# Kernel optimization log

Measured on AMD Instinct MI355X. Metric: run time of the kernel, lower is better.

## Reference

```python
import jax, jax.numpy as jnp
import numpy as np
from jax import lax

_A = -0.75  # PyTorch bicubic coefficient


def _cubic_kernel(x):
    x = np.abs(x)
    return np.where(x <= 1.0, (_A + 2) * x**3 - (_A + 3) * x**2 + 1,
                    np.where(x < 2.0, _A * x**3 - 5 * _A * x**2 + 8 * _A * x - 4 * _A, 0.0))


def _cubic_mat(out_s, in_s):
    # align_corners=True bicubic interpolation matrix [out_s, in_s]
    i = np.arange(out_s)
    s = i * (in_s - 1) / (out_s - 1) if out_s > 1 else np.zeros(out_s)
    f = np.floor(s).astype(np.int64)
    t = s - f
    M = np.zeros((out_s, in_s), dtype=np.float32)
    for off in range(-1, 3):
        idx = np.clip(f + off, 0, in_s - 1)
        np.add.at(M, (i, idx), _cubic_kernel(t - off).astype(np.float32))
    return jnp.asarray(M)


def _bicubic_up(x, out_hw):
    Mh = _cubic_mat(out_hw[0], x.shape[-2])
    Mw = _cubic_mat(out_hw[1], x.shape[-1])
    y = jnp.einsum('Hh,bchw->bcHw', Mh, x)
    return jnp.einsum('Ww,bcHw->bcHW', Mw, y)


def _conv(x, w, b, pad=1):
    y = lax.conv_general_dilated(x, w, (1, 1), [(pad, pad), (pad, pad)],
                                 dimension_numbers=('NCHW', 'OIHW', 'NCHW'))
    return y + b[None, :, None, None]


def _pool(x):
    return lax.reduce_window(x, -jnp.inf, lax.max, (1, 1, 2, 2), (1, 1, 2, 2), 'VALID')


def _features(x, ws):
    # VGG19 feat1 = conv0+relu (64ch, full res); feat2 = conv2..conv14 (256ch, 1/4 res)
    x1 = jax.nn.relu(_conv(x, *ws[0]))
    h = jax.nn.relu(_conv(x1, *ws[1]))
    h = _pool(h)
    h = jax.nn.relu(_conv(h, *ws[2]))
    h = jax.nn.relu(_conv(h, *ws[3]))
    h = _pool(h)
    h = jax.nn.relu(_conv(h, *ws[4]))
    h = jax.nn.relu(_conv(h, *ws[5]))
    h = jax.nn.relu(_conv(h, *ws[6]))
    h = _bicubic_up(h, x1.shape[-2:])  # bicubic, align_corners=True
    return jnp.concatenate([x1, h], axis=1)  # 64 + 256 = 320 channels


def _forward(x_ref, x_template, w0, b0, w2, b2, w5, b5, w7, b7, w10, b10, w12, b12,
             w14, b14, coef_ref, coef_temp, fw1, fb1, fw2, fb2, fw3, fb3):
    ws = [(w0, b0), (w2, b2), (w5, b5), (w7, b7), (w10, b10), (w12, b12), (w14, b14)]
    fref = _features(x_ref, ws)
    ftem = _features(x_template, ws)
    # L2-normalize over channel dim
    fref = fref / (1e-8 + jnp.linalg.norm(fref, axis=1, keepdims=True))
    ftem = ftem / (1e-8 + jnp.linalg.norm(ftem, axis=1, keepdims=True))
    b, c, H, W = fref.shape
    fref = fref.reshape(b, c, H // 2, 2, W // 2, 2).mean(axis=(3, 5))
    # dense correlation volume
    dist = jnp.einsum('bcmn,bcpq->bmnpq', fref, ftem) / 320.0
    m, n, p, q = dist.shape[1:]
    dist = dist.reshape(b, m * n, p * q)
    # dual-axis softmax + sqrt combination (LoFTR-style)
    conf_ref = jax.nn.softmax(coef_ref * dist, axis=-2)
    conf_tmp = jax.nn.softmax(coef_temp * dist, axis=-1)
    confidence = jnp.sqrt(conf_ref * conf_tmp)
    conf_values, _ = lax.top_k(confidence, 5)  # [b, m*n, 5]
    conf = conf_values.reshape(b, m, n, 5).transpose(0, 3, 1, 2)
    # final head (dropout = identity in eval)
    h = jax.nn.relu(_conv(conf, fw1, fb1))
    h = jax.nn.relu(_conv(h, fw2, fb2))
    out = _conv(h, fw3, fb3, pad=0)
    out = _bicubic_up(out, x_ref.shape[-2:])
    return out


def setup_inputs() -> dict:
    key = jax.random.key(0)
    ks = jax.random.split(key, 16)
    B, H, W = 1, 128, 128

    def cw(k, o, i, s):
        return jax.random.normal(k, (o, i, s, s), jnp.float32) * (1.0 / np.sqrt(i * s * s))

    d = {
        'x_ref': jax.random.normal(ks[0], (B, 3, H, W), jnp.float32),
        'x_template': jax.random.normal(ks[1], (B, 3, H, W), jnp.float32),
        'w0': cw(ks[2], 64, 3, 3), 'b0': jnp.zeros((64,), jnp.float32),
        'w2': cw(ks[3], 64, 64, 3), 'b2': jnp.zeros((64,), jnp.float32),
        'w5': cw(ks[4], 128, 64, 3), 'b5': jnp.zeros((128,), jnp.float32),
        'w7': cw(ks[5], 128, 128, 3), 'b7': jnp.zeros((128,), jnp.float32),
        'w10': cw(ks[6], 256, 128, 3), 'b10': jnp.zeros((256,), jnp.float32),
        'w12': cw(ks[7], 256, 256, 3), 'b12': jnp.zeros((256,), jnp.float32),
        'w14': cw(ks[8], 256, 256, 3), 'b14': jnp.zeros((256,), jnp.float32),
        'coef_ref': jnp.float32(1.0), 'coef_temp': jnp.float32(1.0),
        # final head: weights_init_normal -> N(1/3, 0.02)
        'fw1': 1.0 / 3 + 0.02 * jax.random.normal(ks[9], (8, 5, 3, 3), jnp.float32),
        'fb1': 0.02 * jax.random.normal(ks[10], (8,), jnp.float32),
        'fw2': 1.0 / 3 + 0.02 * jax.random.normal(ks[11], (8, 8, 3, 3), jnp.float32),
        'fb2': 0.02 * jax.random.normal(ks[12], (8,), jnp.float32),
        'fw3': 1.0 / 3 + 0.02 * jax.random.normal(ks[13], (1, 8, 1, 1), jnp.float32),
        'fb3': 0.02 * jax.random.normal(ks[14], (1,), jnp.float32),
    }
    return d


def reference(x_ref, x_template, w0, b0, w2, b2, w5, b5, w7, b7, w10, b10, w12, b12,
              w14, b14, coef_ref, coef_temp, fw1, fb1, fw2, fb2, fw3, fb3):
    return _forward(x_ref, x_template, w0, b0, w2, b2, w5, b5, w7, b7, w10, b10,
                    w12, b12, w14, b14, coef_ref, coef_temp, fw1, fb1, fw2, fb2, fw3, fb3)
```

## Files before the change

kernel.cpp:

```cpp
#include <hip/hip_runtime.h>
#include <math.h>

typedef unsigned short ushort_t;
typedef unsigned int uint_t;
typedef __attribute__((ext_vector_type(8))) short bf16x8;
typedef __attribute__((ext_vector_type(4))) float f32x4;

#define FSTRIDE ((size_t)16384 * 320)
#define TSTRIDE ((size_t)16384 * 64)

__device__ inline ushort_t f2bf(float f) {
    union { float f; uint_t u; } x; x.f = f;
    uint_t r = x.u + 0x7fffu + ((x.u >> 16) & 1u);
    return (ushort_t)(r >> 16);
}
__device__ inline float bf2f(ushort_t h) {
    union { uint_t u; float f; } x; x.u = ((uint_t)h) << 16;
    return x.f;
}
__device__ inline float bflo(uint_t u) {
    union { uint_t u; float f; } x; x.u = u << 16; return x.f;
}
__device__ inline float bfhi(uint_t u) {
    union { uint_t u; float f; } x; x.u = u & 0xffff0000u; return x.f;
}
__device__ inline uint_t cvtpk_bf16(float lo, float hi) {
    uint_t r;
    asm volatile("v_cvt_pk_bf16_f32 %0, %1, %2" : "=v"(r) : "v"(lo), "v"(hi));
    return r;
}
__device__ inline void gload16(const void* g, void* l) {
    __builtin_amdgcn_global_load_lds(
        (const __attribute__((address_space(1))) void*)g,
        (__attribute__((address_space(3))) void*)l, 16, 0, 0);
}

__global__ void wtrans_k(const float* __restrict__ w, ushort_t* __restrict__ wT, int CO, int CI)
{
    int idx = blockIdx.x * 256 + threadIdx.x;
    if (idx >= CO * CI * 9) return;
    int tap = idx % 9;
    int rem = idx / 9;
    int ci = rem % CI;
    int co = rem / CI;
    wT[((size_t)tap * CO + co) * CI + ci] = f2bf(w[idx]);
}

__global__ __launch_bounds__(256) void conv0_k(const float* __restrict__ x0, const float* __restrict__ x1,
                                               const float* __restrict__ w,
                                               const float* __restrict__ b, ushort_t* __restrict__ F)
{
    const float* x = blockIdx.y ? x1 : x0;
    F += (size_t)blockIdx.y * FSTRIDE;
    int co = threadIdx.x & 63;
    int p = blockIdx.x * 4 + (threadIdx.x >> 6);
    int y = p >> 7, xx = p & 127;
    float acc = b[co];
#pragma unroll
    for (int ci = 0; ci < 3; ++ci) {
#pragma unroll
        for (int t = 0; t < 9; ++t) {
            int dy = t / 3 - 1, dx = t % 3 - 1;
            int yy = y + dy, xc = xx + dx;
            if ((unsigned)yy < 128u && (unsigned)xc < 128u) {
                acc += x[ci * 16384 + yy * 128 + xc] * w[co * 27 + ci * 9 + t];
            }
        }
    }
    F[(size_t)p * 320 + co] = f2bf(fmaxf(acc, 0.f));
}

template<int CI>
__global__ __launch_bounds__(256) void conv_mfma_k(
    const ushort_t* __restrict__ in, int ldin, int inoff, size_t inImgStride,
    const ushort_t* __restrict__ wT, const float* __restrict__ bias,
    ushort_t* __restrict__ out, int ldout, int outoff, size_t outImgStride,
    int H, int W, int CO)
{
    in += (size_t)blockIdx.z * inImgStride;
    out += (size_t)blockIdx.z * outImgStride;
    const int tid = threadIdx.x;
    const int lane = tid & 63, wid = tid >> 6;
    const int wr = wid >> 1, wc = wid & 1;
    const int m0 = blockIdx.x * 64;
    const int n0 = blockIdx.y * 64;
    const int fr = lane & 15;
    const int fo = (lane >> 4) << 3;

    size_t abase[2];
    unsigned vmask[2];
#pragma unroll
    for (int mi = 0; mi < 2; ++mi) {
        int p = m0 + wr * 32 + mi * 16 + fr;
        int y = p / W, x = p % W;
        abase[mi] = (size_t)p * ldin + inoff + fo;
        unsigned vm = 0;
#pragma unroll
        for (int t = 0; t < 9; ++t) {
            int dy = t / 3 - 1, dx = t % 3 - 1;
            if ((unsigned)(y + dy) < (unsigned)H && (unsigned)(x + dx) < (unsigned)W) vm |= 1u << t;
        }
        vmask[mi] = vm;
    }

    f32x4 zero = {0.f, 0.f, 0.f, 0.f};
    f32x4 acc[2][2] = {{zero, zero}, {zero, zero}};
    const bf16x8 zz = {0, 0, 0, 0, 0, 0, 0, 0};

    for (int t = 0; t < 9; ++t) {
        int toff = ((t / 3 - 1) * W + (t % 3 - 1)) * ldin;
        bool v0 = (vmask[0] >> t) & 1u;
        bool v1 = (vmask[1] >> t) & 1u;
        const ushort_t* wp0 = wT + ((size_t)(t * CO + n0 + wc * 32 + fr)) * CI + fo;
        const ushort_t* wp1 = wp0 + (size_t)16 * CI;
#pragma unroll
        for (int kc = 0; kc < CI / 32; ++kc) {
            int k0 = kc * 32;
            bf16x8 a0 = v0 ? *(const bf16x8*)(in + abase[0] + toff + k0) : zz;
            bf16x8 a1 = v1 ? *(const bf16x8*)(in + abase[1] + toff + k0) : zz;
            bf16x8 b0 = *(const bf16x8*)(wp0 + k0);
            bf16x8 b1 = *(const bf16x8*)(wp1 + k0);
            acc[0][0] = __builtin_amdgcn_mfma_f32_16x16x32_bf16(b0, a0, acc[0][0], 0, 0, 0);
            acc[0][1] = __builtin_amdgcn_mfma_f32_16x16x32_bf16(b1, a0, acc[0][1], 0, 0, 0);
            acc[1][0] = __builtin_amdgcn_mfma_f32_16x16x32_bf16(b0, a1, acc[1][0], 0, 0, 0);
            acc[1][1] = __builtin_amdgcn_mfma_f32_16x16x32_bf16(b1, a1, acc[1][1], 0, 0, 0);
        }
    }

#pragma unroll
    for (int mi = 0; mi < 2; ++mi) {
#pragma unroll
        for (int ni = 0; ni < 2; ++ni) {
            int pix = m0 + wr * 32 + mi * 16 + (lane & 15);
            int ch = n0 + wc * 32 + ni * 16 + ((lane >> 4) << 2);
            float4 bv = *(const float4*)(bias + ch);
            float r0 = fmaxf(acc[mi][ni][0] + bv.x, 0.f);
            float r1 = fmaxf(acc[mi][ni][1] + bv.y, 0.f);
            float r2 = fmaxf(acc[mi][ni][2] + bv.z, 0.f);
            float r3 = fmaxf(acc[mi][ni][3] + bv.w, 0.f);
            uint2 pk;
            pk.x = (uint_t)f2bf(r0) | ((uint_t)f2bf(r1) << 16);
            pk.y = (uint_t)f2bf(r2) | ((uint_t)f2bf(r3) << 16);
            *(uint2*)(out + (size_t)pix * ldout + outoff + ch) = pk;
        }
    }
}

template<int CI>
__global__ __launch_bounds__(64) void conv_mfma1w_k(
    const ushort_t* __restrict__ in, int ldin, size_t inImgStride,
    const ushort_t* __restrict__ wT, const float* __restrict__ bias,
    ushort_t* __restrict__ out, int ldout, size_t outImgStride,
    int H, int W, int CO)
{
    in += (size_t)blockIdx.z * inImgStride;
    out += (size_t)blockIdx.z * outImgStride;
    const int lane = threadIdx.x;
    const int m0 = blockIdx.x * 32;
    const int n0 = blockIdx.y * 32;
    const int fr = lane & 15;
    const int fo = (lane >> 4) << 3;

    size_t abase[2];
    unsigned vmask[2];
#pragma unroll
    for (int mi = 0; mi < 2; ++mi) {
        int p = m0 + mi * 16 + fr;
        int y = p / W, x = p % W;
        abase[mi] = (size_t)p * ldin + fo;
        unsigned vm = 0;
#pragma unroll
        for (int t = 0; t < 9; ++t) {
            int dy = t / 3 - 1, dx = t % 3 - 1;
            if ((unsigned)(y + dy) < (unsigned)H && (unsigned)(x + dx) < (unsigned)W) vm |= 1u << t;
        }
        vmask[mi] = vm;
    }

    f32x4 zero = {0.f, 0.f, 0.f, 0.f};
    f32x4 acc[2][2] = {{zero, zero}, {zero, zero}};
    const bf16x8 zz = {0, 0, 0, 0, 0, 0, 0, 0};

    for (int t = 0; t < 9; ++t) {
        int toff = ((t / 3 - 1) * W + (t % 3 - 1)) * ldin;
        bool v0 = (vmask[0] >> t) & 1u;
        bool v1 = (vmask[1] >> t) & 1u;
        const ushort_t* wp0 = wT + ((size_t)(t * CO + n0 + fr)) * CI + fo;
        const ushort_t* wp1 = wp0 + (size_t)16 * CI;
#pragma unroll
        for (int kc = 0; kc < CI / 32; ++kc) {
            int k0 = kc * 32;
            bf16x8 a0 = v0 ? *(const bf16x8*)(in + abase[0] + toff + k0) : zz;
            bf16x8 a1 = v1 ? *(const bf16x8*)(in + abase[1] + toff + k0) : zz;
            bf16x8 b0 = *(const bf16x8*)(wp0 + k0);
            bf16x8 b1 = *(const bf16x8*)(wp1 + k0);
            acc[0][0] = __builtin_amdgcn_mfma_f32_16x16x32_bf16(b0, a0, acc[0][0], 0, 0, 0);
            acc[0][1] = __builtin_amdgcn_mfma_f32_16x16x32_bf16(b1, a0, acc[0][1], 0, 0, 0);
            acc[1][0] = __builtin_amdgcn_mfma_f32_16x16x32_bf16(b0, a1, acc[1][0], 0, 0, 0);
            acc[1][1] = __builtin_amdgcn_mfma_f32_16x16x32_bf16(b1, a1, acc[1][1], 0, 0, 0);
        }
    }

#pragma unroll
    for (int mi = 0; mi < 2; ++mi) {
#pragma unroll
        for (int ni = 0; ni < 2; ++ni) {
            int pix = m0 + mi * 16 + (lane & 15);
            int ch = n0 + ni * 16 + ((lane >> 4) << 2);
            float4 bv = *(const float4*)(bias + ch);
            float r0 = fmaxf(acc[mi][ni][0] + bv.x, 0.f);
            float r1 = fmaxf(acc[mi][ni][1] + bv.y, 0.f);
            float r2 = fmaxf(acc[mi][ni][2] + bv.z, 0.f);
            float r3 = fmaxf(acc[mi][ni][3] + bv.w, 0.f);
            uint2 pk;
            pk.x = (uint_t)f2bf(r0) | ((uint_t)f2bf(r1) << 16);
            pk.y = (uint_t)f2bf(r2) | ((uint_t)f2bf(r3) << 16);
            *(uint2*)(out + (size_t)pix * ldout + ch) = pk;
        }
    }
}

__global__ void maxpool_nhwc_k(const ushort_t* __restrict__ in, ushort_t* __restrict__ out,
                               int C, int Hi, int Wi)
{
    in += (size_t)blockIdx.y * TSTRIDE;
    out += (size_t)blockIdx.y * TSTRIDE;
    int idx = blockIdx.x * 256 + threadIdx.x;
    int CG = C >> 3;
    int Wo = Wi >> 1, Ho = Hi >> 1;
    if (idx >= Ho * Wo * CG) return;
    int cg = idx % CG;
    int p = idx / CG;
    int y = p / Wo, x = p % Wo;
    const ushort_t* ip = in + ((size_t)(2 * y) * Wi + 2 * x) * C + cg * 8;
    bf16x8 v0 = *(const bf16x8*)(ip);
    bf16x8 v1 = *(const bf16x8*)(ip + C);
    bf16x8 v2 = *(const bf16x8*)(ip + (size_t)Wi * C);
    bf16x8 v3 = *(const bf16x8*)(ip + (size_t)Wi * C + C);
    bf16x8 r;
#pragma unroll
    for (int j = 0; j < 8; ++j) {
        float m = fmaxf(fmaxf(bf2f((ushort_t)v0[j]), bf2f((ushort_t)v1[j])),
                        fmaxf(bf2f((ushort_t)v2[j]), bf2f((ushort_t)v3[j])));
        r[j] = (short)f2bf(m);
    }
    *(bf16x8*)(out + (size_t)p * C + cg * 8) = r;
}

__device__ inline void cubw(float t, float* w) {
    float x0 = 1.f + t, x2 = 1.f - t, x3 = 2.f - t;
    w[0] = ((-0.75f*x0 + 3.75f)*x0 - 6.f)*x0 + 3.f;
    w[1] = (1.25f*t - 2.25f)*t*t + 1.f;
    w[2] = (1.25f*x2 - 2.25f)*x2*x2 + 1.f;
    w[3] = ((-0.75f*x3 + 3.75f)*x3 - 6.f)*x3 + 3.f;
}

__global__ __launch_bounds__(256) void bicubic_nhwc_k(const ushort_t* __restrict__ in, ushort_t* __restrict__ F)
{
    in += (size_t)blockIdx.y * TSTRIDE;
    F += (size_t)blockIdx.y * FSTRIDE;
    int idx = blockIdx.x * 256 + threadIdx.x;
    int cg = idx & 31;
    int p = idx >> 5;
    int Y = p >> 7, X = p & 127;
    float sy = (float)Y * (31.f / 127.f);
    float sx = (float)X * (31.f / 127.f);
    int fy = (int)floorf(sy), fx = (int)floorf(sx);
    float ty = sy - (float)fy, tx = sx - (float)fx;
    float wy[4], wx[4];
    cubw(ty, wy); cubw(tx, wx);
    float a[8] = {0.f, 0.f, 0.f, 0.f, 0.f, 0.f, 0.f, 0.f};
#pragma unroll
    for (int i = 0; i < 4; ++i) {
        int yy = min(max(fy - 1 + i, 0), 31);
#pragma unroll
        for (int j = 0; j < 4; ++j) {
            int xx = min(max(fx - 1 + j, 0), 31);
            float w = wy[i] * wx[j];
            bf16x8 v = *(const bf16x8*)(in + ((size_t)yy * 32 + xx) * 256 + cg * 8);
#pragma unroll
            for (int e = 0; e < 8; ++e) a[e] += w * bf2f((ushort_t)v[e]);
        }
    }
    bf16x8 r;
#pragma unroll
    for (int e = 0; e < 8; ++e) r[e] = (short)f2bf(a[e]);
    *(bf16x8*)(F + (size_t)p * 320 + 64 + cg * 8) = r;
}

__global__ __launch_bounds__(256) void norm_k(ushort_t* __restrict__ F)
{
    int lane = threadIdx.x & 63;
    int p = blockIdx.x * 4 + (threadIdx.x >> 6);
    ushort_t* rp = F + (size_t)p * 320;
    bool act = lane < 40;
    bf16x8 v = {0, 0, 0, 0, 0, 0, 0, 0};
    float ss = 0.f;
    if (act) {
        v = *(const bf16x8*)(rp + lane * 8);
#pragma unroll
        for (int e = 0; e < 8; ++e) { float f = bf2f((ushort_t)v[e]); ss += f * f; }
    }
#pragma unroll
    for (int off = 32; off > 0; off >>= 1) ss += __shfl_xor(ss, off);
    float inv = 1.f / (1e-8f + sqrtf(ss));
    if (act) {
#pragma unroll
        for (int e = 0; e < 8; ++e) v[e] = (short)f2bf(bf2f((ushort_t)v[e]) * inv);
        *(bf16x8*)(rp + lane * 8) = v;
    }
}

__global__ void pool_ref_nhwc_k(const ushort_t* __restrict__ F, ushort_t* __restrict__ A)
{
    int idx = blockIdx.x * 256 + threadIdx.x;
    if (idx >= 4096 * 40) return;
    int cg = idx % 40;
    int m = idx / 40;
    int y = m >> 6, x = m & 63;
    const ushort_t* ip = F + ((size_t)(2 * y) * 128 + 2 * x) * 320 + cg * 8;
    bf16x8 v0 = *(const bf16x8*)(ip);
    bf16x8 v1 = *(const bf16x8*)(ip + 320);
    bf16x8 v2 = *(const bf16x8*)(ip + 128 * 320);
    bf16x8 v3 = *(const bf16x8*)(ip + 128 * 320 + 320);
    bf16x8 r;
#pragma unroll
    for (int j = 0; j < 8; ++j) {
        float s = bf2f((ushort_t)v0[j]) + bf2f((ushort_t)v1[j]) + bf2f((ushort_t)v2[j]) + bf2f((ushort_t)v3[j]);
        r[j] = (short)f2bf(0.25f * s);
    }
    *(bf16x8*)(A + (size_t)m * 320 + cg * 8) = r;
}

__global__ __launch_bounds__(256) void gemm_corr_k(
    const ushort_t* __restrict__ A, const ushort_t* __restrict__ B, ushort_t* __restrict__ D,
    const float* __restrict__ coefr, const float* __restrict__ coeft,
    float* __restrict__ rpsum, float* __restrict__ cpsum)
{
    __shared__ ushort_t lA[128 * 32];
    __shared__ ushort_t lB[128 * 32];
    __shared__ float cl[2][128];
    __shared__ float rl[2][128];
    const int tid = threadIdx.x;
    const int lane = tid & 63;
    const int wid = tid >> 6;
    const int wr = wid >> 1, wc = wid & 1;
    const int m0 = blockIdx.y * 128, n0 = blockIdx.x * 128;
    const int fr = lane & 15;
    const int fo = (lane >> 4) << 3;
    const int srow = tid >> 2;
    const int scol = (tid & 3) << 3;

    const ushort_t* Ag0 = A + (size_t)(m0 + srow) * 320 + scol;
    const ushort_t* Ag1 = Ag0 + (size_t)64 * 320;
    const ushort_t* Bg0 = B + (size_t)(n0 + srow) * 320 + scol;
    const ushort_t* Bg1 = Bg0 + (size_t)64 * 320;
    ushort_t* lA0 = lA + wid * 512;
    ushort_t* lA1 = lA + 2048 + wid * 512;
    ushort_t* lB0 = lB + wid * 512;
    ushort_t* lB1 = lB + 2048 + wid * 512;

    f32x4 zero = {0.f, 0.f, 0.f, 0.f};
    f32x4 acc[4][4];
#pragma unroll
    for (int i = 0; i < 4; ++i)
#pragma unroll
        for (int j = 0; j < 4; ++j) acc[i][j] = zero;

    for (int k0 = 0; k0 < 320; k0 += 32) {
        gload16(Ag0 + k0, lA0);
        gload16(Ag1 + k0, lA1);
        gload16(Bg0 + k0, lB0);
        gload16(Bg1 + k0, lB1);
        __syncthreads();
        bf16x8 af[4], bfr[4];
#pragma unroll
        for (int mi = 0; mi < 4; ++mi)
            af[mi] = *(const bf16x8*)&lA[(wr * 64 + mi * 16 + fr) * 32 + fo];
#pragma unroll
        for (int ni = 0; ni < 4; ++ni)
            bfr[ni] = *(const bf16x8*)&lB[(wc * 64 + ni * 16 + fr) * 32 + fo];
#pragma unroll
        for (int mi = 0; mi < 4; ++mi)
#pragma unroll
            for (int ni = 0; ni < 4; ++ni)
                acc[mi][ni] = __builtin_amdgcn_mfma_f32_16x16x32_bf16(bfr[ni], af[mi], acc[mi][ni], 0, 0, 0);
        __syncthreads();
    }

    const float s = 1.0f / 320.0f;
    const float cr = coefr[0], ct = coeft[0];
    const bool sameCoef = (cr == ct);
    float rpx[4] = {0.f, 0.f, 0.f, 0.f};
    float cpx[4][4];
#pragma unroll
    for (int ni = 0; ni < 4; ++ni)
#pragma unroll
        for (int r = 0; r < 4; ++r) cpx[ni][r] = 0.f;

    const int mrow = lane & 15;
    const int ng = (lane >> 4) << 2;
#pragma unroll
    for (int mi = 0; mi < 4; ++mi) {
        int m = m0 + wr * 64 + mi * 16 + mrow;
        ushort_t* drow = D + (size_t)m * 16384;
#pragma unroll
        for (int ni = 0; ni < 4; ++ni) {
            int n = n0 + wc * 64 + ni * 16 + ng;
            float d0 = acc[mi][ni][0] * s;
            float d1 = acc[mi][ni][1] * s;
            float d2 = acc[mi][ni][2] * s;
            float d3 = acc[mi][ni][3] * s;
            uint2 pk;
            pk.x = cvtpk_bf16(d0, d1);
            pk.y = cvtpk_bf16(d2, d3);
            *(uint2*)(drow + n) = pk;
            float e0 = __expf(cr * d0), e1 = __expf(cr * d1);
            float e2 = __expf(cr * d2), e3 = __expf(cr * d3);
            cpx[ni][0] += e0; cpx[ni][1] += e1; cpx[ni][2] += e2; cpx[ni][3] += e3;
            if (sameCoef) {
                rpx[mi] += e0 + e1 + e2 + e3;
            } else {
                rpx[mi] += __expf(ct * d0) + __expf(ct * d1) + __expf(ct * d2) + __expf(ct * d3);
            }
        }
    }
#pragma unroll
    for (int mi = 0; mi < 4; ++mi) {
        rpx[mi] += __shfl_xor(rpx[mi], 16);
        rpx[mi] += __shfl_xor(rpx[mi], 32);
    }
    if (lane < 16) {
#pragma unroll
        for (int mi = 0; mi < 4; ++mi)
            rl[wc][wr * 64 + mi * 16 + lane] = rpx[mi];
    }
#pragma unroll
    for (int ni = 0; ni < 4; ++ni)
#pragma unroll
        for (int r = 0; r < 4; ++r) {
            cpx[ni][r] += __shfl_xor(cpx[ni][r], 1);
            cpx[ni][r] += __shfl_xor(cpx[ni][r], 2);
            cpx[ni][r] += __shfl_xor(cpx[ni][r], 4);
            cpx[ni][r] += __shfl_xor(cpx[ni][r], 8);
        }
    if ((lane & 15) == 0) {
        int g = lane >> 4;
#pragma unroll
        for (int ni = 0; ni < 4; ++ni)
#pragma unroll
            for (int r = 0; r < 4; ++r)
                cl[wr][wc * 64 + ni * 16 + g * 4 + r] = cpx[ni][r];
    }
    __syncthreads();
    if (tid < 128) {
        cpsum[(size_t)blockIdx.y * 16384 + n0 + tid] = cl[0][tid] + cl[1][tid];
        rpsum[(size_t)blockIdx.x * 4096 + m0 + tid] = rl[0][tid] + rl[1][tid];
    }
}

__global__ void colfin_k(const float* __restrict__ cpsum, float* __restrict__ lc)
{
    int j = blockIdx.x * 256 + threadIdx.x;
    float s = 0.f;
#pragma unroll
    for (int k = 0; k < 32; ++k) s += cpsum[(size_t)k * 16384 + j];
    lc[j] = -0.5f * __logf(s);
}
__global__ void rowfin_k(const float* __restrict__ rpsum, float* __restrict__ invr)
{
    int m = blockIdx.x * 256 + threadIdx.x;
    float s = 0.f;
#pragma unroll
    for (int k = 0; k < 128; ++k) s += rpsum[(size_t)k * 4096 + m];
    invr[m] = rsqrtf(s);
}

#define INS5(w_) { float w = (w_); float mx; \
    mx = fmaxf(w, t0); w = fminf(w, t0); t0 = mx; \
    mx = fmaxf(w, t1); w = fminf(w, t1); t1 = mx; \
    mx = fmaxf(w, t2); w = fminf(w, t2); t2 = mx; \
    mx = fmaxf(w, t3); w = fminf(w, t3); t3 = mx; \
    t4 = fmaxf(w, t4); }

__global__ __launch_bounds__(256) void row_topk_k(
    const ushort_t* __restrict__ Dist, const float* __restrict__ lc,
    const float* __restrict__ invr,
    const float* __restrict__ coefr, const float* __restrict__ coeft,
    float* __restrict__ conf5)
{
    int wid = threadIdx.x >> 6, lane = threadIdx.x & 63;
    int row = blockIdx.x * 4 + wid;
    float hc = 0.5f * (coefr[0] + coeft[0]);
    const ushort_t* rp = Dist + (size_t)row * 16384;

    float t0 = -1e30f, t1 = -1e30f, t2 = -1e30f, t3 = -1e30f, t4 = -1e30f;
    for (int i = 0; i < 32; ++i) {
        int col = (i * 64 + lane) * 8;
        uint4 u = *(const uint4*)(rp + col);
        float4 l0 = *(const float4*)(lc + col);
        float4 l1 = *(const float4*)(lc + col + 4);
        INS5(fmaf(hc, bflo(u.x), l0.x));
        INS5(fmaf(hc, bfhi(u.x), l0.y));
        INS5(fmaf(hc, bflo(u.y), l0.z));
        INS5(fmaf(hc, bfhi(u.y), l0.w));
        INS5(fmaf(hc, bflo(u.z), l1.x));
        INS5(fmaf(hc, bfhi(u.z), l1.y));
        INS5(fmaf(hc, bflo(u.w), l1.z));
        INS5(fmaf(hc, bfhi(u.w), l1.w));
    }
#pragma unroll
    for (int off = 1; off < 64; off <<= 1) {
        float o0 = __shfl_xor(t0, off), o1 = __shfl_xor(t1, off), o2 = __shfl_xor(t2, off);
        float o3 = __shfl_xor(t3, off), o4 = __shfl_xor(t4, off);
        INS5(o0); INS5(o1); INS5(o2); INS5(o3); INS5(o4);
    }
    if (lane == 0) {
        float iv = invr[row];
        conf5[0 * 4096 + row] = __expf(t0) * iv;
        conf5[1 * 4096 + row] = __expf(t1) * iv;
        conf5[2 * 4096 + row] = __expf(t2) * iv;
        conf5[3 * 4096 + row] = __expf(t3) * iv;
        conf5[4 * 4096 + row] = __expf(t4) * iv;
    }
}

__global__ void conv3x3_k(const float* __restrict__ in, const float* __restrict__ wgt,
                          const float* __restrict__ bias, float* __restrict__ out,
                          int Cin, int H, int W, int relu)
{
    int p = blockIdx.x * 256 + threadIdx.x;
    int HW = H * W;
    if (p >= HW) return;
    int co0 = blockIdx.y * 8;
    int y = p / W, x = p - y * W;
    float acc0 = bias[co0+0], acc1 = bias[co0+1], acc2 = bias[co0+2], acc3 = bias[co0+3];
    float acc4 = bias[co0+4], acc5 = bias[co0+5], acc6 = bias[co0+6], acc7 = bias[co0+7];
    bool ym = y > 0, yp = y < H-1, xm = x > 0, xp = x < W-1;
    for (int ci = 0; ci < Cin; ++ci) {
        const float* ip = in + (size_t)ci * HW + p;
        float v0 = (ym && xm) ? ip[-W-1] : 0.f;
        float v1 = (ym)       ? ip[-W]   : 0.f;
        float v2 = (ym && xp) ? ip[-W+1] : 0.f;
        float v3 = (xm)       ? ip[-1]   : 0.f;
        float v4 =              ip[0];
        float v5 = (xp)       ? ip[1]    : 0.f;
        float v6 = (yp && xm) ? ip[W-1]  : 0.f;
        float v7 = (yp)       ? ip[W]    : 0.f;
        float v8 = (yp && xp) ? ip[W+1]  : 0.f;
        const float* wp = wgt + ((size_t)co0 * Cin + ci) * 9;
        size_t ws = (size_t)Cin * 9;
#define CACC(q, a) { const float* wq = wp + q * ws; \
        a += wq[0]*v0 + wq[1]*v1 + wq[2]*v2 + wq[3]*v3 + wq[4]*v4 \
           + wq[5]*v5 + wq[6]*v6 + wq[7]*v7 + wq[8]*v8; }
        CACC(0, acc0) CACC(1, acc1) CACC(2, acc2) CACC(3, acc3)
        CACC(4, acc4) CACC(5, acc5) CACC(6, acc6) CACC(7, acc7)
#undef CACC
    }
#define CW(q, a) { float r = a; if (relu) r = fmaxf(r, 0.f); out[(size_t)(co0+q)*HW + p] = r; }
    CW(0, acc0) CW(1, acc1) CW(2, acc2) CW(3, acc3)
    CW(4, acc4) CW(5, acc5) CW(6, acc6) CW(7, acc7)
#undef CW
}

__global__ void bicubic_k(const float* __restrict__ in, float* __restrict__ out,
                          int C, int Hin, int Win, int Hout, int Wout)
{
    int idx = blockIdx.x * 256 + threadIdx.x;
    int total = C * Hout * Wout;
    if (idx >= total) return;
    int X = idx % Wout;
    int Y = (idx / Wout) % Hout;
    int c = idx / (Wout * Hout);
    float sy = (float)Y * (float)(Hin - 1) / (float)(Hout - 1);
    float sx = (float)X * (float)(Win - 1) / (float)(Wout - 1);
    int fy = (int)floorf(sy), fx = (int)floorf(sx);
    float ty = sy - (float)fy, tx = sx - (float)fx;
    float wy[4], wx[4];
    cubw(ty, wy); cubw(tx, wx);
    const float* ip = in + (size_t)c * Hin * Win;
    float acc = 0.f;
#pragma unroll
    for (int i = 0; i < 4; ++i) {
        int yy = min(max(fy - 1 + i, 0), Hin - 1);
        float ra = 0.f;
#pragma unroll
        for (int j = 0; j < 4; ++j) {
            int xx = min(max(fx - 1 + j, 0), Win - 1);
            ra += wx[j] * ip[yy * Win + xx];
        }
        acc += wy[i] * ra;
    }
    out[idx] = acc;
}

__global__ void conv1x1_k(const float* __restrict__ in, const float* __restrict__ w,
                          const float* __restrict__ b, float* __restrict__ out, int Cin, int HW)
{
    int p = blockIdx.x * 256 + threadIdx.x;
    if (p >= HW) return;
    float a = b[0];
    for (int c = 0; c < Cin; ++c) a += w[c] * in[(size_t)c * HW + p];
    out[p] = a;
}

extern "C" void kernel_launch(void* const* d_in, const int* in_sizes, int n_in,
                              void* d_out, int out_size, void* d_ws, size_t ws_size,
                              hipStream_t stream)
{
    const float* x_ref = (const float*)d_in[0];
    const float* x_tem = (const float*)d_in[1];
    const float* w0  = (const float*)d_in[2];   const float* b0  = (const float*)d_in[3];
    const float* w2  = (const float*)d_in[4];   const float* b2  = (const float*)d_in[5];
    const float* w5  = (const float*)d_in[6];   const float* b5  = (const float*)d_in[7];
    const float* w7  = (const float*)d_in[8];   const float* b7  = (const float*)d_in[9];
    const float* w10 = (const float*)d_in[10];  const float* b10 = (const float*)d_in[11];
    const float* w12 = (const float*)d_in[12];  const float* b12 = (const float*)d_in[13];
    const float* w14 = (const float*)d_in[14];  const float* b14 = (const float*)d_in[15];
    const float* coefr = (const float*)d_in[16];
    const float* coeft = (const float*)d_in[17];
    const float* fw1 = (const float*)d_in[18];  const float* fb1 = (const float*)d_in[19];
    const float* fw2 = (const float*)d_in[20];  const float* fb2 = (const float*)d_in[21];
    const float* fw3 = (const float*)d_in[22];  const float* fb3 = (const float*)d_in[23];
    float* out = (float*)d_out;

    char* wsp = (char*)d_ws;
    auto alloc = [&](size_t bytes) { char* p = wsp; wsp += (bytes + 255) & ~(size_t)255; return p; };
    ushort_t* F     = (ushort_t*)alloc(2 * FSTRIDE * 2);
    ushort_t* t1    = (ushort_t*)alloc(2 * TSTRIDE * 2);
    ushort_t* t2    = (ushort_t*)alloc(2 * TSTRIDE * 2);
    ushort_t* wT2   = (ushort_t*)alloc((size_t)64 * 64 * 9 * 2);
    ushort_t* wT5   = (ushort_t*)alloc((size_t)128 * 64 * 9 * 2);
    ushort_t* wT7   = (ushort_t*)alloc((size_t)128 * 128 * 9 * 2);
    ushort_t* wT10  = (ushort_t*)alloc((size_t)256 * 128 * 9 * 2);
    ushort_t* wT12  = (ushort_t*)alloc((size_t)256 * 256 * 9 * 2);
    ushort_t* wT14  = (ushort_t*)alloc((size_t)256 * 256 * 9 * 2);
    ushort_t* Abuf  = (ushort_t*)alloc((size_t)4096 * 320 * 2);
    ushort_t* dist  = (ushort_t*)alloc((size_t)4096 * 16384 * 2);
    float*    rpsum = (float*)alloc((size_t)128 * 4096 * 4);
    float*    cpsum = (float*)alloc((size_t)32 * 16384 * 4);
    float*    lc    = (float*)alloc(16384 * 4);
    float*    invr  = (float*)alloc(4096 * 4);
    float*    conf5 = (float*)alloc(5 * 4096 * 4);
    float*    h1    = (float*)alloc(8 * 4096 * 4);
    float*    h2    = (float*)alloc(8 * 4096 * 4);
    float*    out64 = (float*)alloc(4096 * 4);
    (void)ws_size; (void)n_in; (void)in_sizes; (void)out_size;

    wtrans_k<<<(64*64*9 + 255)/256, 256, 0, stream>>>(w2, wT2, 64, 64);
    wtrans_k<<<(128*64*9 + 255)/256, 256, 0, stream>>>(w5, wT5, 128, 64);
    wtrans_k<<<(128*128*9 + 255)/256, 256, 0, stream>>>(w7, wT7, 128, 128);
    wtrans_k<<<(256*128*9 + 255)/256, 256, 0, stream>>>(w10, wT10, 256, 128);
    wtrans_k<<<(256*256*9 + 255)/256, 256, 0, stream>>>(w12, wT12, 256, 256);
    wtrans_k<<<(256*256*9 + 255)/256, 256, 0, stream>>>(w14, wT14, 256, 256);

    conv0_k<<<dim3(4096, 2), 256, 0, stream>>>(x_ref, x_tem, w0, b0, F);
    conv_mfma_k<64><<<dim3(256, 1, 2), 256, 0, stream>>>(F, 320, 0, FSTRIDE, wT2, b2, t1, 64, 0, TSTRIDE, 128, 128, 64);
    maxpool_nhwc_k<<<dim3(128, 2), 256, 0, stream>>>(t1, t2, 64, 128, 128);
    conv_mfma_k<64><<<dim3(64, 2, 2), 256, 0, stream>>>(t2, 64, 0, TSTRIDE, wT5, b5, t1, 128, 0, TSTRIDE, 64, 64, 128);
    conv_mfma_k<128><<<dim3(64, 2, 2), 256, 0, stream>>>(t1, 128, 0, TSTRIDE, wT7, b7, t2, 128, 0, TSTRIDE, 64, 64, 128);
    maxpool_nhwc_k<<<dim3(64, 2), 256, 0, stream>>>(t2, t1, 128, 64, 64);
    conv_mfma1w_k<128><<<dim3(32, 8, 2), 64, 0, stream>>>(t1, 128, TSTRIDE, wT10, b10, t2, 256, TSTRIDE, 32, 32, 256);
    conv_mfma1w_k<256><<<dim3(32, 8, 2), 64, 0, stream>>>(t2, 256, TSTRIDE, wT12, b12, t1, 256, TSTRIDE, 32, 32, 256);
    conv_mfma1w_k<256><<<dim3(32, 8, 2), 64, 0, stream>>>(t1, 256, TSTRIDE, wT14, b14, t2, 256, TSTRIDE, 32, 32, 256);
    bicubic_nhwc_k<<<dim3(2048, 2), 256, 0, stream>>>(t2, F);
    norm_k<<<8192, 256, 0, stream>>>(F);

    pool_ref_nhwc_k<<<640, 256, 0, stream>>>(F, Abuf);

    gemm_corr_k<<<dim3(128, 32), 256, 0, stream>>>(Abuf, F + FSTRIDE, dist, coefr, coeft, rpsum, cpsum);

    colfin_k<<<64, 256, 0, stream>>>(cpsum, lc);
    rowfin_k<<<16, 256, 0, stream>>>(rpsum, invr);

    row_topk_k<<<1024, 256, 0, stream>>>(dist, lc, invr, coefr, coeft, conf5);

    conv3x3_k<<<dim3(16, 1), 256, 0, stream>>>(conf5, fw1, fb1, h1, 5, 64, 64, 1);
    conv3x3_k<<<dim3(16, 1), 256, 0, stream>>>(h1, fw2, fb2, h2, 8, 64, 64, 1);
    conv1x1_k<<<16, 256, 0, stream>>>(h2, fw3, fb3, out64, 8, 4096);
    bicubic_k<<<64, 256, 0, stream>>>(out64, out, 1, 64, 64, 128, 128);
}
```

Measured before the change: 409.7 us.

## Fuse small kernels, prefetch GEMM tiles via registers, early-exit top-k insert

```diff
diff --git a/kernel.cpp b/kernel.cpp
--- a/kernel.cpp
+++ b/kernel.cpp
@@ -29,21 +29,26 @@
     asm volatile("v_cvt_pk_bf16_f32 %0, %1, %2" : "=v"(r) : "v"(lo), "v"(hi));
     return r;
 }
-__device__ inline void gload16(const void* g, void* l) {
-    __builtin_amdgcn_global_load_lds(
-        (const __attribute__((address_space(1))) void*)g,
-        (__attribute__((address_space(3))) void*)l, 16, 0, 0);
-}
-
-__global__ void wtrans_k(const float* __restrict__ w, ushort_t* __restrict__ wT, int CO, int CI)
-{
-    int idx = blockIdx.x * 256 + threadIdx.x;
+
+struct WT6 {
+    const float* src[6];
+    ushort_t* dst[6];
+    int co[6], ci[6];
+    int off[6];
+};
+__global__ void wtrans6_k(WT6 a)
+{
+    int b = blockIdx.x, seg = 0;
+#pragma unroll
+    for (int s = 1; s < 6; ++s) if (b >= a.off[s]) seg = s;
+    int idx = (b - a.off[seg]) * 256 + threadIdx.x;
+    int CO = a.co[seg], CI = a.ci[seg];
     if (idx >= CO * CI * 9) return;
     int tap = idx % 9;
     int rem = idx / 9;
     int ci = rem % CI;
     int co = rem / CI;
-    wT[((size_t)tap * CO + co) * CI + ci] = f2bf(w[idx]);
+    a.dst[seg][((size_t)tap * CO + co) * CI + ci] = f2bf(a.src[seg][idx]);
 }
 
 __global__ __launch_bounds__(256) void conv0_k(const float* __restrict__ x0, const float* __restrict__ x1,
@@ -255,13 +260,12 @@
     w[3] = ((-0.75f*x3 + 3.75f)*x3 - 6.f)*x3 + 3.f;
 }
 
-__global__ __launch_bounds__(256) void bicubic_nhwc_k(const ushort_t* __restrict__ in, ushort_t* __restrict__ F)
+__global__ __launch_bounds__(256) void upnorm_k(const ushort_t* __restrict__ in, ushort_t* __restrict__ F)
 {
     in += (size_t)blockIdx.y * TSTRIDE;
     F += (size_t)blockIdx.y * FSTRIDE;
-    int idx = blockIdx.x * 256 + threadIdx.x;
-    int cg = idx & 31;
-    int p = idx >> 5;
+    int wid = threadIdx.x >> 6, lane = threadIdx.x & 63;
+    int p = blockIdx.x * 4 + wid;
     int Y = p >> 7, X = p & 127;
     float sy = (float)Y * (31.f / 127.f);
     float sx = (float)X * (31.f / 127.f);
@@ -269,7 +273,7 @@
     float ty = sy - (float)fy, tx = sx - (float)fx;
     float wy[4], wx[4];
     cubw(ty, wy); cubw(tx, wx);
-    float a[8] = {0.f, 0.f, 0.f, 0.f, 0.f, 0.f, 0.f, 0.f};
+    float a0 = 0.f, a1 = 0.f, a2 = 0.f, a3 = 0.f;
 #pragma unroll
     for (int i = 0; i < 4; ++i) {
         int yy = min(max(fy - 1 + i, 0), 31);
@@ -277,38 +281,22 @@
         for (int j = 0; j < 4; ++j) {
             int xx = min(max(fx - 1 + j, 0), 31);
             float w = wy[i] * wx[j];
-            bf16x8 v = *(const bf16x8*)(in + ((size_t)yy * 32 + xx) * 256 + cg * 8);
-#pragma unroll
-            for (int e = 0; e < 8; ++e) a[e] += w * bf2f((ushort_t)v[e]);
-        }
-    }
-    bf16x8 r;
-#pragma unroll
-    for (int e = 0; e < 8; ++e) r[e] = (short)f2bf(a[e]);
-    *(bf16x8*)(F + (size_t)p * 320 + 64 + cg * 8) = r;
-}
-
-__global__ __launch_bounds__(256) void norm_k(ushort_t* __restrict__ F)
-{
-    int lane = threadIdx.x & 63;
-    int p = blockIdx.x * 4 + (threadIdx.x >> 6);
-    ushort_t* rp = F + (size_t)p * 320;
-    bool act = lane < 40;
-    bf16x8 v = {0, 0, 0, 0, 0, 0, 0, 0};
-    float ss = 0.f;
-    if (act) {
-        v = *(const bf16x8*)(rp + lane * 8);
-#pragma unroll
-        for (int e = 0; e < 8; ++e) { float f = bf2f((ushort_t)v[e]); ss += f * f; }
-    }
+            uint2 v = *(const uint2*)(in + ((size_t)yy * 32 + xx) * 256 + lane * 4);
+            a0 += w * bflo(v.x); a1 += w * bfhi(v.x);
+            a2 += w * bflo(v.y); a3 += w * bfhi(v.y);
+        }
+    }
+    float v0 = bf2f(f2bf(a0)), v1 = bf2f(f2bf(a1)), v2 = bf2f(f2bf(a2)), v3 = bf2f(f2bf(a3));
+    float c0 = bf2f(F[(size_t)p * 320 + lane]);
+    float ss = c0 * c0 + v0 * v0 + v1 * v1 + v2 * v2 + v3 * v3;
 #pragma unroll
     for (int off = 32; off > 0; off >>= 1) ss += __shfl_xor(ss, off);
     float inv = 1.f / (1e-8f + sqrtf(ss));
-    if (act) {
-#pragma unroll
-        for (int e = 0; e < 8; ++e) v[e] = (short)f2bf(bf2f((ushort_t)v[e]) * inv);
-        *(bf16x8*)(rp + lane * 8) = v;
-    }
+    F[(size_t)p * 320 + lane] = f2bf(c0 * inv);
+    uint2 pk;
+    pk.x = (uint_t)f2bf(v0 * inv) | ((uint_t)f2bf(v1 * inv) << 16);
+    pk.y = (uint_t)f2bf(v2 * inv) | ((uint_t)f2bf(v3 * inv) << 16);
+    *(uint2*)(F + (size_t)p * 320 + 64 + lane * 4) = pk;
 }
 
 __global__ void pool_ref_nhwc_k(const ushort_t* __restrict__ F, ushort_t* __restrict__ A)
@@ -355,10 +343,6 @@
     const ushort_t* Ag1 = Ag0 + (size_t)64 * 320;
     const ushort_t* Bg0 = B + (size_t)(n0 + srow) * 320 + scol;
     const ushort_t* Bg1 = Bg0 + (size_t)64 * 320;
-    ushort_t* lA0 = lA + wid * 512;
-    ushort_t* lA1 = lA + 2048 + wid * 512;
-    ushort_t* lB0 = lB + wid * 512;
-    ushort_t* lB1 = lB + 2048 + wid * 512;
 
     f32x4 zero = {0.f, 0.f, 0.f, 0.f};
     f32x4 acc[4][4];
@@ -367,11 +351,27 @@
 #pragma unroll
         for (int j = 0; j < 4; ++j) acc[i][j] = zero;
 
-    for (int k0 = 0; k0 < 320; k0 += 32) {
-        gload16(Ag0 + k0, lA0);
-        gload16(Ag1 + k0, lA1);
-        gload16(Bg0 + k0, lB0);
-        gload16(Bg1 + k0, lB1);
+    uint4 ra0[2], ra1[2], rb0[2], rb1[2];
+    ra0[0] = *(const uint4*)(Ag0);
+    ra1[0] = *(const uint4*)(Ag1);
+    rb0[0] = *(const uint4*)(Bg0);
+    rb1[0] = *(const uint4*)(Bg1);
+
+#pragma unroll
+    for (int t = 0; t < 10; ++t) {
+        const int cs = t & 1, ns = cs ^ 1;
+        __syncthreads();
+        *(uint4*)&lA[srow * 32 + scol] = ra0[cs];
+        *(uint4*)&lA[(64 + srow) * 32 + scol] = ra1[cs];
+        *(uint4*)&lB[srow * 32 + scol] = rb0[cs];
+        *(uint4*)&lB[(64 + srow) * 32 + scol] = rb1[cs];
+        if (t < 9) {
+            int kk = 32 * (t + 1);
+            ra0[ns] = *(const uint4*)(Ag0 + kk);
+            ra1[ns] = *(const uint4*)(Ag1 + kk);
+            rb0[ns] = *(const uint4*)(Bg0 + kk);
+            rb1[ns] = *(const uint4*)(Bg1 + kk);
+        }
         __syncthreads();
         bf16x8 af[4], bfr[4];
 #pragma unroll
@@ -385,7 +385,6 @@
 #pragma unroll
             for (int ni = 0; ni < 4; ++ni)
                 acc[mi][ni] = __builtin_amdgcn_mfma_f32_16x16x32_bf16(bfr[ni], af[mi], acc[mi][ni], 0, 0, 0);
-        __syncthreads();
     }
 
     const float s = 1.0f / 320.0f;
@@ -459,21 +458,23 @@
     }
 }
 
-__global__ void colfin_k(const float* __restrict__ cpsum, float* __restrict__ lc)
-{
-    int j = blockIdx.x * 256 + threadIdx.x;
-    float s = 0.f;
-#pragma unroll
-    for (int k = 0; k < 32; ++k) s += cpsum[(size_t)k * 16384 + j];
-    lc[j] = -0.5f * __logf(s);
-}
-__global__ void rowfin_k(const float* __restrict__ rpsum, float* __restrict__ invr)
-{
-    int m = blockIdx.x * 256 + threadIdx.x;
-    float s = 0.f;
-#pragma unroll
-    for (int k = 0; k < 128; ++k) s += rpsum[(size_t)k * 4096 + m];
-    invr[m] = rsqrtf(s);
+__global__ void finboth_k(const float* __restrict__ cpsum, const float* __restrict__ rpsum,
+                          float* __restrict__ lc, float* __restrict__ invr)
+{
+    int b = blockIdx.x;
+    if (b < 64) {
+        int j = b * 256 + threadIdx.x;
+        float s = 0.f;
+#pragma unroll
+        for (int k = 0; k < 32; ++k) s += cpsum[(size_t)k * 16384 + j];
+        lc[j] = -0.5f * __logf(s);
+    } else {
+        int m = (b - 64) * 256 + threadIdx.x;
+        float s = 0.f;
+#pragma unroll
+        for (int k = 0; k < 128; ++k) s += rpsum[(size_t)k * 4096 + m];
+        invr[m] = rsqrtf(s);
+    }
 }
 
 #define INS5(w_) { float w = (w_); float mx; \
@@ -500,14 +501,20 @@
         uint4 u = *(const uint4*)(rp + col);
         float4 l0 = *(const float4*)(lc + col);
         float4 l1 = *(const float4*)(lc + col + 4);
-        INS5(fmaf(hc, bflo(u.x), l0.x));
-        INS5(fmaf(hc, bfhi(u.x), l0.y));
-        INS5(fmaf(hc, bflo(u.y), l0.z));
-        INS5(fmaf(hc, bfhi(u.y), l0.w));
-        INS5(fmaf(hc, bflo(u.z), l1.x));
-        INS5(fmaf(hc, bfhi(u.z), l1.y));
-        INS5(fmaf(hc, bflo(u.w), l1.z));
-        INS5(fmaf(hc, bfhi(u.w), l1.w));
+        float k0 = fmaf(hc, bflo(u.x), l0.x);
+        float k1 = fmaf(hc, bfhi(u.x), l0.y);
+        float k2 = fmaf(hc, bflo(u.y), l0.z);
+        float k3 = fmaf(hc, bfhi(u.y), l0.w);
+        float k4 = fmaf(hc, bflo(u.z), l1.x);
+        float k5 = fmaf(hc, bfhi(u.z), l1.y);
+        float k6 = fmaf(hc, bflo(u.w), l1.z);
+        float k7 = fmaf(hc, bfhi(u.w), l1.w);
+        float m8 = fmaxf(fmaxf(fmaxf(k0, k1), fmaxf(k2, k3)),
+                         fmaxf(fmaxf(k4, k5), fmaxf(k6, k7)));
+        if (m8 > t4) {
+            INS5(k0); INS5(k1); INS5(k2); INS5(k3);
+            INS5(k4); INS5(k5); INS5(k6); INS5(k7);
+        }
     }
 #pragma unroll
     for (int off = 1; off < 64; off <<= 1) {
@@ -563,6 +570,41 @@
 #undef CW
 }
 
+__global__ void head2_k(const float* __restrict__ in, const float* __restrict__ wgt,
+                        const float* __restrict__ bias, const float* __restrict__ w3,
+                        const float* __restrict__ b3, float* __restrict__ out64)
+{
+    int p = blockIdx.x * 256 + threadIdx.x;
+    int y = p >> 6, x = p & 63;
+    float acc[8];
+#pragma unroll
+    for (int c = 0; c < 8; ++c) acc[c] = bias[c];
+    bool ym = y > 0, yp = y < 63, xm = x > 0, xp = x < 63;
+#pragma unroll
+    for (int ci = 0; ci < 8; ++ci) {
+        const float* ip = in + ci * 4096 + p;
+        float v0 = (ym && xm) ? ip[-65] : 0.f;
+        float v1 = (ym)       ? ip[-64] : 0.f;
+        float v2 = (ym && xp) ? ip[-63] : 0.f;
+        float v3 = (xm)       ? ip[-1]  : 0.f;
+        float v4 =              ip[0];
+        float v5 = (xp)       ? ip[1]   : 0.f;
+        float v6 = (yp && xm) ? ip[63]  : 0.f;
+        float v7 = (yp)       ? ip[64]  : 0.f;
+        float v8 = (yp && xp) ? ip[65]  : 0.f;
+#pragma unroll
+        for (int co = 0; co < 8; ++co) {
+            const float* wq = wgt + ((size_t)co * 8 + ci) * 9;
+            acc[co] += wq[0]*v0 + wq[1]*v1 + wq[2]*v2 + wq[3]*v3 + wq[4]*v4
+                     + wq[5]*v5 + wq[6]*v6 + wq[7]*v7 + wq[8]*v8;
+        }
+    }
+    float o = b3[0];
+#pragma unroll
+    for (int c = 0; c < 8; ++c) o += w3[c] * fmaxf(acc[c], 0.f);
+    out64[p] = o;
+}
+
 __global__ void bicubic_k(const float* __restrict__ in, float* __restrict__ out,
                           int C, int Hin, int Win, int Hout, int Wout)
 {
@@ -592,16 +634,6 @@
         acc += wy[i] * ra;
     }
     out[idx] = acc;
-}
-
-__global__ void conv1x1_k(const float* __restrict__ in, const float* __restrict__ w,
-                          const float* __restrict__ b, float* __restrict__ out, int Cin, int HW)
-{
-    int p = blockIdx.x * 256 + threadIdx.x;
-    if (p >= HW) return;
-    float a = b[0];
-    for (int c = 0; c < Cin; ++c) a += w[c] * in[(size_t)c * HW + p];
-    out[p] = a;
 }
 
 extern "C" void kernel_launch(void* const* d_in, const int* in_sizes, int n_in,
@@ -643,16 +675,19 @@
     float*    invr  = (float*)alloc(4096 * 4);
     float*    conf5 = (float*)alloc(5 * 4096 * 4);
     float*    h1    = (float*)alloc(8 * 4096 * 4);
-    float*    h2    = (float*)alloc(8 * 4096 * 4);
     float*    out64 = (float*)alloc(4096 * 4);
     (void)ws_size; (void)n_in; (void)in_sizes; (void)out_size;
 
-    wtrans_k<<<(64*64*9 + 255)/256, 256, 0, stream>>>(w2, wT2, 64, 64);
-    wtrans_k<<<(128*64*9 + 255)/256, 256, 0, stream>>>(w5, wT5, 128, 64);
-    wtrans_k<<<(128*128*9 + 255)/256, 256, 0, stream>>>(w7, wT7, 128, 128);
-    wtrans_k<<<(256*128*9 + 255)/256, 256, 0, stream>>>(w10, wT10, 256, 128);
-    wtrans_k<<<(256*256*9 + 255)/256, 256, 0, stream>>>(w12, wT12, 256, 256);
-    wtrans_k<<<(256*256*9 + 255)/256, 256, 0, stream>>>(w14, wT14, 256, 256);
+    WT6 wt;
+    wt.src[0] = w2;  wt.dst[0] = wT2;  wt.co[0] = 64;  wt.ci[0] = 64;
+    wt.src[1] = w5;  wt.dst[1] = wT5;  wt.co[1] = 128; wt.ci[1] = 64;
+    wt.src[2] = w7;  wt.dst[2] = wT7;  wt.co[2] = 128; wt.ci[2] = 128;
+    wt.src[3] = w10; wt.dst[3] = wT10; wt.co[3] = 256; wt.ci[3] = 128;
+    wt.src[4] = w12; wt.dst[4] = wT12; wt.co[4] = 256; wt.ci[4] = 256;
+    wt.src[5] = w14; wt.dst[5] = wT14; wt.co[5] = 256; wt.ci[5] = 256;
+    int nblk = 0;
+    for (int s = 0; s < 6; ++s) { wt.off[s] = nblk; nblk += (wt.co[s] * wt.ci[s] * 9 + 255) / 256; }
+    wtrans6_k<<<nblk, 256, 0, stream>>>(wt);
 
     conv0_k<<<dim3(4096, 2), 256, 0, stream>>>(x_ref, x_tem, w0, b0, F);
     conv_mfma_k<64><<<dim3(256, 1, 2), 256, 0, stream>>>(F, 320, 0, FSTRIDE, wT2, b2, t1, 64, 0, TSTRIDE, 128, 128, 64);
@@ -663,20 +698,17 @@
     conv_mfma1w_k<128><<<dim3(32, 8, 2), 64, 0, stream>>>(t1, 128, TSTRIDE, wT10, b10, t2, 256, TSTRIDE, 32, 32, 256);
     conv_mfma1w_k<256><<<dim3(32, 8, 2), 64, 0, stream>>>(t2, 256, TSTRIDE, wT12, b12, t1, 256, TSTRIDE, 32, 32, 256);
     conv_mfma1w_k<256><<<dim3(32, 8, 2), 64, 0, stream>>>(t1, 256, TSTRIDE, wT14, b14, t2, 256, TSTRIDE, 32, 32, 256);
-    bicubic_nhwc_k<<<dim3(2048, 2), 256, 0, stream>>>(t2, F);
-    norm_k<<<8192, 256, 0, stream>>>(F);
+    upnorm_k<<<dim3(4096, 2), 256, 0, stream>>>(t2, F);
 
     pool_ref_nhwc_k<<<640, 256, 0, stream>>>(F, Abuf);
 
     gemm_corr_k<<<dim3(128, 32), 256, 0, stream>>>(Abuf, F + FSTRIDE, dist, coefr, coeft, rpsum, cpsum);
 
-    colfin_k<<<64, 256, 0, stream>>>(cpsum, lc);
-    rowfin_k<<<16, 256, 0, stream>>>(rpsum, invr);
+    finboth_k<<<80, 256, 0, stream>>>(cpsum, rpsum, lc, invr);
 
     row_topk_k<<<1024, 256, 0, stream>>>(dist, lc, invr, coefr, coeft, conf5);
 
     conv3x3_k<<<dim3(16, 1), 256, 0, stream>>>(conf5, fw1, fb1, h1, 5, 64, 64, 1);
-    conv3x3_k<<<dim3(16, 1), 256, 0, stream>>>(h1, fw2, fb2, h2, 8, 64, 64, 1);
-    conv1x1_k<<<16, 256, 0, stream>>>(h2, fw3, fb3, out64, 8, 4096);
+    head2_k<<<16, 256, 0, stream>>>(h1, fw2, fb2, fw3, fb3, out64);
     bicubic_k<<<64, 256, 0, stream>>>(out64, out, 1, 64, 64, 128, 128);
 }
```

Result: slower. 543.4 us (+32.6%).
